# Kernel tuning notes

Measured on AMD Instinct MI355X. Metric: run time of the kernel, lower is better.

## Reference

```python
import jax, jax.numpy as jnp
import numpy as np

NEG_SLOPE = 0.2  # PyG GATConv default leaky_relu slope


def gat_conv(x, src, dst, W, a_src, a_dst, b, heads, out_dim):
    """PyG-style GATConv (add_self_loops already applied to src/dst, concat=True)."""
    N = x.shape[0]
    h = (x @ W).reshape(N, heads, out_dim)              # [N,H,D]
    alpha_s = jnp.sum(h * a_src, axis=-1)               # [N,H]
    alpha_d = jnp.sum(h * a_dst, axis=-1)               # [N,H]
    e = jax.nn.leaky_relu(alpha_s[src] + alpha_d[dst], NEG_SLOPE)  # [E,H]
    # segment softmax over destination node neighborhoods
    m = jax.lax.stop_gradient(jax.ops.segment_max(e, dst, num_segments=N))
    ex = jnp.exp(e - m[dst])
    denom = jax.ops.segment_sum(ex, dst, num_segments=N)
    alpha = ex / denom[dst]                              # [E,H]
    msg = h[src] * alpha[..., None]                      # [E,H,D]
    out = jax.ops.segment_sum(msg, dst, num_segments=N)  # [N,H,D]
    return out.reshape(N, heads * out_dim) + b


def setup_inputs() -> dict:
    key = jax.random.key(0)
    ks = jax.random.split(key, 12)
    N, E, C_IN, HID, HEADS, C_OUT = 50000, 800000, 128, 64, 4, 64
    x = jax.random.normal(ks[0], (N, C_IN), dtype=jnp.float32)
    edge_index = jax.random.randint(ks[1], (2, E), 0, N, dtype=jnp.int32)
    s1 = 1.0 / np.sqrt(C_IN)
    s2 = 1.0 / np.sqrt(HID * HEADS)
    return {
        "x": x,
        "edge_index": edge_index,
        "W1": jax.random.normal(ks[2], (C_IN, HEADS * HID), jnp.float32) * s1,
        "a_src1": jax.random.normal(ks[3], (HEADS, HID), jnp.float32) * s1,
        "a_dst1": jax.random.normal(ks[4], (HEADS, HID), jnp.float32) * s1,
        "b1": jnp.zeros((HEADS * HID,), jnp.float32),
        "W2": jax.random.normal(ks[5], (HEADS * HID, C_OUT), jnp.float32) * s2,
        "a_src2": jax.random.normal(ks[6], (1, C_OUT), jnp.float32) * s2,
        "a_dst2": jax.random.normal(ks[7], (1, C_OUT), jnp.float32) * s2,
        "b2": jnp.zeros((C_OUT,), jnp.float32),
    }


def reference(x, edge_index, W1, a_src1, a_dst1, b1, W2, a_src2, a_dst2, b2):
    N = x.shape[0]
    loop = jnp.arange(N, dtype=edge_index.dtype)
    src = jnp.concatenate([edge_index[0], loop])  # add self-loops (PyG default)
    dst = jnp.concatenate([edge_index[1], loop])
    # dropout layers are identity in eval mode
    h = gat_conv(x, src, dst, W1, a_src1, a_dst1, b1, heads=4, out_dim=64)
    h = jax.nn.relu(h)
    out = gat_conv(h, src, dst, W2, a_src2, a_dst2, b2, heads=1, out_dim=64)
    return out  # [N, out_channels]
```

## Files before the change

### kernel.cpp

```cpp
#include <hip/hip_runtime.h>
#include <math.h>

#define LEAKY 0.2f
#define SB 256
#define FTILE 4096

typedef _Float16 half2v __attribute__((ext_vector_type(2)));
typedef _Float16 half4 __attribute__((ext_vector_type(4)));
typedef _Float16 half8 __attribute__((ext_vector_type(8)));
typedef float f32x4 __attribute__((ext_vector_type(4)));

static inline int ceil_div(int a, int b) { return (a + b - 1) / b; }

__device__ __forceinline__ int PERM(int p) {
  int q = p & 63;
  return (p & ~63) | (((q & 3) << 4) | (q >> 2));
}

__global__ __launch_bounds__(256) void k_zero(int4* __restrict__ buf, int n4) {
  int i = blockIdx.x * 256 + threadIdx.x;
  if (i < n4) buf[i] = make_int4(0, 0, 0, 0);
}

__global__ __launch_bounds__(256) void k_fillA(const int* __restrict__ ei,
                                               int* __restrict__ bcnt,
                                               int2* __restrict__ pairs,
                                               int NE, int N, int chunk, int cap) {
  __shared__ int hist[256], base[256], cnt2[256];
  int t = threadIdx.x;
  hist[t] = 0;
  cnt2[t] = 0;
  __syncthreads();
  int ET = NE + N;
  int e0 = blockIdx.x * FTILE;
  int sv[16], dv[16];
#pragma unroll
  for (int j = 0; j < 16; ++j) {
    int e = e0 + t + 256 * j;
    if (e < ET) {
      sv[j] = (e < NE) ? ei[e] : (e - NE);
      dv[j] = (e < NE) ? ei[NE + e] : (e - NE);
      atomicAdd(&hist[dv[j] / chunk], 1);
    } else {
      dv[j] = -1;
    }
  }
  __syncthreads();
  if (hist[t] > 0) base[t] = t * cap + atomicAdd(&bcnt[t], hist[t]);
  __syncthreads();
#pragma unroll
  for (int j = 0; j < 16; ++j) {
    if (dv[j] >= 0) {
      int b = dv[j] / chunk;
      int r = atomicAdd(&cnt2[b], 1);
      pairs[base[b] + r] = make_int2(dv[j], sv[j]);
    }
  }
}

__global__ __launch_bounds__(256) void k_bscan(const int* __restrict__ bcnt,
                                               int* __restrict__ bpre,
                                               int* __restrict__ off, int N) {
  __shared__ int s[256];
  int t = threadIdx.x;
  int v = bcnt[t];
  s[t] = v;
  __syncthreads();
  for (int o = 1; o < 256; o <<= 1) {
    int u = (t >= o) ? s[t - o] : 0;
    __syncthreads();
    s[t] += u;
    __syncthreads();
  }
  bpre[t] = s[t] - v;
  if (t == 255) off[N] = s[255];
}

__global__ __launch_bounds__(256) void k_fillB2(const int2* __restrict__ pairs,
                                                const int* __restrict__ bcnt,
                                                const int* __restrict__ bpre,
                                                int* __restrict__ off,
                                                int* __restrict__ csr, int N,
                                                int chunk, int cap) {
  __shared__ int hist[256], cur[256];
  int b = blockIdx.x, t = threadIdx.x;
  int node0 = b * chunk;
  hist[t] = 0;
  __syncthreads();
  int i0 = b * cap, i1 = i0 + bcnt[b];
  for (int i = i0 + t; i < i1; i += 256)
    atomicAdd(&hist[pairs[i].x - node0], 1);
  __syncthreads();
  int v = hist[t];
  for (int o = 1; o < 256; o <<= 1) {
    int u = (t >= o) ? hist[t - o] : 0;
    __syncthreads();
    hist[t] += u;
    __syncthreads();
  }
  int ex = hist[t] - v + bpre[b];
  if (t < chunk && node0 + t < N) off[node0 + t] = ex;
  cur[t] = ex;
  __syncthreads();
  for (int i = i0 + t; i < i1; i += 256) {
    int2 pr = pairs[i];
    int pos = atomicAdd(&cur[pr.x - node0], 1);
    csr[pos] = pr.y;
  }
}

__global__ __launch_bounds__(256) void k_prep(const float* __restrict__ W1,
                                              const float* __restrict__ W2,
                                              const float* __restrict__ a_src1,
                                              const float* __restrict__ a_dst1,
                                              const float* __restrict__ a_src2,
                                              const float* __restrict__ a_dst2,
                                              const float* __restrict__ b1,
                                              _Float16* __restrict__ w1hf,
                                              _Float16* __restrict__ w2f,
                                              float* __restrict__ wt1s,
                                              float* __restrict__ wt1d,
                                              float* __restrict__ b1p) {
  int idx = blockIdx.x * 256 + threadIdx.x;
  if (idx < 32768) {
    int i = idx & 7, l = (idx >> 3) & 63, ct = (idx >> 9) & 3, ks = (idx >> 11) & 3,
        h = idx >> 13;
    int k = 32 * ks + 8 * (l >> 4) + i;
    int col = h * 64 + 16 * ct + (l & 15);
    w1hf[idx] = (_Float16)W1[k * 256 + col];
    return;
  }
  int i2 = idx - 32768;
  if (i2 < 16384) {
    int i = i2 & 7, l = (i2 >> 3) & 63, ct = (i2 >> 9) & 3, ks = i2 >> 11;
    int kp = 32 * ks + 8 * (l >> 4) + i;
    int col = 16 * ct + (l & 15);
    w2f[i2] = (_Float16)W2[PERM(kp) * 64 + col];
    return;
  }
  int i3 = i2 - 16384;
  if (i3 < 512) {
    int h = i3 & 3, k = i3 >> 2;
    float ss = 0.f, sd = 0.f;
    for (int d = 0; d < 64; ++d) {
      float wv = W1[k * 256 + h * 64 + d];
      ss = fmaf(wv, a_src1[h * 64 + d], ss);
      sd = fmaf(wv, a_dst1[h * 64 + d], sd);
    }
    wt1s[i3] = ss;
    wt1d[i3] = sd;
    return;
  }
  int i4 = i3 - 512;
  if (i4 < 256) b1p[i4] = b1[PERM(i4)];
}

__global__ __launch_bounds__(256) void k_logits1(const float* __restrict__ x,
                                                 const float* __restrict__ wt1s,
                                                 const float* __restrict__ wt1d,
                                                 _Float16* __restrict__ x16,
                                                 float* __restrict__ as1,
                                                 float* __restrict__ ad1, int N) {
  int w = threadIdx.x >> 6, l = threadIdx.x & 63;
  int n = blockIdx.x * 4 + w;
  if (n >= N) return;
  float2 xv = *reinterpret_cast<const float2*>(x + (size_t)n * 128 + 2 * l);
  half2v xh;
  xh[0] = (_Float16)xv.x;
  xh[1] = (_Float16)xv.y;
  *reinterpret_cast<half2v*>(x16 + (size_t)n * 128 + 2 * l) = xh;
  float4 w0s = reinterpret_cast<const float4*>(wt1s)[2 * l];
  float4 w1s = reinterpret_cast<const float4*>(wt1s)[2 * l + 1];
  float4 w0d = reinterpret_cast<const float4*>(wt1d)[2 * l];
  float4 w1d = reinterpret_cast<const float4*>(wt1d)[2 * l + 1];
  float sa[4], sd[4];
  sa[0] = xv.x * w0s.x + xv.y * w1s.x;
  sa[1] = xv.x * w0s.y + xv.y * w1s.y;
  sa[2] = xv.x * w0s.z + xv.y * w1s.z;
  sa[3] = xv.x * w0s.w + xv.y * w1s.w;
  sd[0] = xv.x * w0d.x + xv.y * w1d.x;
  sd[1] = xv.x * w0d.y + xv.y * w1d.y;
  sd[2] = xv.x * w0d.z + xv.y * w1d.z;
  sd[3] = xv.x * w0d.w + xv.y * w1d.w;
#pragma unroll
  for (int o = 1; o <= 32; o <<= 1) {
#pragma unroll
    for (int h = 0; h < 4; ++h) {
      sa[h] += __shfl_xor(sa[h], o, 64);
      sd[h] += __shfl_xor(sd[h], o, 64);
    }
  }
  if (l == 0) {
#pragma unroll
    for (int h = 0; h < 4; ++h) {
      as1[n * 4 + h] = sa[h];
      ad1[n * 4 + h] = sd[h];
    }
  }
}

__global__ __launch_bounds__(256) void k_alpha1(const float* __restrict__ as1,
                                                const float* __restrict__ ad1,
                                                const int* __restrict__ off,
                                                const int* __restrict__ csr,
                                                _Float16* __restrict__ alpha,
                                                float* __restrict__ linv1, int N) {
  int w = threadIdx.x >> 6, lane = threadIdx.x & 63;
  int n = blockIdx.x * 4 + w;
  if (n >= N) return;
  int eidx = lane >> 2, h = lane & 3;
  float adv = ad1[n * 4 + h];
  int e0 = off[n], e1 = off[n + 1];
  float m = -INFINITY;
  for (int base = e0; base < e1; base += 16) {
    int idx = base + eidx;
    if (idx < e1) {
      int s = csr[idx];
      float t = as1[s * 4 + h] + adv;
      t = t > 0.f ? t : LEAKY * t;
      m = fmaxf(m, t);
    }
  }
#pragma unroll
  for (int o = 4; o <= 32; o <<= 1) m = fmaxf(m, __shfl_xor(m, o, 64));
  float lp = 0.f;
  for (int base = e0; base < e1; base += 16) {
    int idx = base + eidx;
    if (idx < e1) {
      int s = csr[idx];
      float t = as1[s * 4 + h] + adv;
      t = t > 0.f ? t : LEAKY * t;
      float p = __expf(t - m);
      alpha[(size_t)idx * 4 + h] = (_Float16)p;
      lp += p;
    }
  }
#pragma unroll
  for (int o = 4; o <= 32; o <<= 1) lp += __shfl_xor(lp, o, 64);
  if (lane < 4) linv1[n * 4 + h] = 1.f / lp;
}

__global__ __launch_bounds__(256) void k_xagg(const _Float16* __restrict__ x16,
                                              const _Float16* __restrict__ alpha,
                                              const float* __restrict__ linv1,
                                              const int* __restrict__ off,
                                              const int* __restrict__ csr,
                                              _Float16* __restrict__ xagg, int N) {
  int w = threadIdx.x >> 6, l = threadIdx.x & 63;
  int n = blockIdx.x * 4 + w;
  if (n >= N) return;
  int slot = l >> 4, kq = l & 15;
  int e0 = off[n], e1 = off[n + 1];
  half2v acc[4][4];
#pragma unroll
  for (int h = 0; h < 4; ++h)
#pragma unroll
    for (int j = 0; j < 4; ++j) acc[h][j] = (half2v){(_Float16)0.f, (_Float16)0.f};
  const _Float16 zero16 = (_Float16)0.f;
  for (int base = e0; base < e1; base += 16) {
#pragma unroll
    for (int u = 0; u < 4; ++u) {
      int e = base + 4 * u + slot;
      int ec = min(e, e1 - 1);
      int src = csr[ec];
      half4 al = *reinterpret_cast<const half4*>(alpha + (size_t)ec * 4);
      if (e >= e1) al = (half4){zero16, zero16, zero16, zero16};
      half8 hv = *reinterpret_cast<const half8*>(x16 + (size_t)src * 128 + 8 * kq);
      half2v xp[4];
      xp[0] = (half2v){hv[0], hv[1]};
      xp[1] = (half2v){hv[2], hv[3]};
      xp[2] = (half2v){hv[4], hv[5]};
      xp[3] = (half2v){hv[6], hv[7]};
#pragma unroll
      for (int h = 0; h < 4; ++h) {
        half2v ah = (half2v){al[h], al[h]};
#pragma unroll
        for (int j = 0; j < 4; ++j) acc[h][j] = ah * xp[j] + acc[h][j];
      }
    }
  }
#pragma unroll
  for (int h = 0; h < 4; ++h)
#pragma unroll
    for (int j = 0; j < 4; ++j) {
      int v0 = __shfl_xor(__builtin_bit_cast(int, acc[h][j]), 16, 64);
      acc[h][j] = acc[h][j] + __builtin_bit_cast(half2v, v0);
      int v1 = __shfl_xor(__builtin_bit_cast(int, acc[h][j]), 32, 64);
      acc[h][j] = acc[h][j] + __builtin_bit_cast(half2v, v1);
    }
  if (slot == 0) {
    float4 linv = *reinterpret_cast<const float4*>(linv1 + n * 4);
    float rin[4] = {linv.x, linv.y, linv.z, linv.w};
#pragma unroll
    for (int h = 0; h < 4; ++h) {
      half8 o;
#pragma unroll
      for (int j = 0; j < 4; ++j) {
        o[2 * j] = (_Float16)((float)acc[h][j][0] * rin[h]);
        o[2 * j + 1] = (_Float16)((float)acc[h][j][1] * rin[h]);
      }
      *reinterpret_cast<half8*>(xagg + (size_t)n * 512 + h * 128 + 8 * kq) = o;
    }
  }
}

__global__ __launch_bounds__(256) void k_gemm12(const _Float16* __restrict__ xagg,
                                                const _Float16* __restrict__ w1hf,
                                                const _Float16* __restrict__ w2f,
                                                const float* __restrict__ b1p,
                                                const float* __restrict__ a_src2,
                                                const float* __restrict__ a_dst2,
                                                _Float16* __restrict__ h2p,
                                                float* __restrict__ as2,
                                                float* __restrict__ ad2, int N) {
  __shared__ _Float16 hs[64 * 256];
  int w = threadIdx.x >> 6, l = threadIdx.x & 63;
  int n0 = blockIdx.x * 64 + 16 * w;
  int lrow = l & 15, lgrp = l >> 4;
  int arow = min(n0 + lrow, N - 1);
  f32x4 acc1[4][4];
#pragma unroll
  for (int h = 0; h < 4; ++h)
#pragma unroll
    for (int ct = 0; ct < 4; ++ct) acc1[h][ct] = (f32x4){0.f, 0.f, 0.f, 0.f};
#pragma unroll
  for (int h = 0; h < 4; ++h) {
#pragma unroll
    for (int ks = 0; ks < 4; ++ks) {
      half8 af = *reinterpret_cast<const half8*>(xagg + (size_t)arow * 512 + h * 128 +
                                                 32 * ks + 8 * lgrp);
      const half8* bp =
          reinterpret_cast<const half8*>(w1hf) + (size_t)((h * 4 + ks) * 4) * 64 + l;
#pragma unroll
      for (int ct = 0; ct < 4; ++ct) {
        half8 bf = bp[ct * 64];
        acc1[h][ct] = __builtin_amdgcn_mfma_f32_16x16x32_f16(af, bf, acc1[h][ct], 0, 0, 0);
      }
    }
  }
  int lr0 = 16 * w + 4 * lgrp;
#pragma unroll
  for (int h = 0; h < 4; ++h) {
    float4 bv = *reinterpret_cast<const float4*>(b1p + h * 64 + lrow * 4);
#pragma unroll
    for (int r = 0; r < 4; ++r) {
      int row = lr0 + r;
      half4 o;
      o[0] = (_Float16)fmaxf(acc1[h][0][r] + bv.x, 0.f);
      o[1] = (_Float16)fmaxf(acc1[h][1][r] + bv.y, 0.f);
      o[2] = (_Float16)fmaxf(acc1[h][2][r] + bv.z, 0.f);
      o[3] = (_Float16)fmaxf(acc1[h][3][r] + bv.w, 0.f);
      int ba = row * 512 + ((h * 128 + lrow * 8) ^ ((row & 7) << 4));
      *reinterpret_cast<half4*>(reinterpret_cast<char*>(hs) + ba) = o;
    }
  }
  __syncthreads();
  int arow2 = 16 * w + lrow;
  f32x4 acc2[4];
#pragma unroll
  for (int ct = 0; ct < 4; ++ct) acc2[ct] = (f32x4){0.f, 0.f, 0.f, 0.f};
#pragma unroll
  for (int ks = 0; ks < 8; ++ks) {
    int ba = arow2 * 512 + ((64 * ks + 16 * lgrp) ^ ((arow2 & 7) << 4));
    half8 af = *reinterpret_cast<const half8*>(reinterpret_cast<const char*>(hs) + ba);
    const half8* bp = reinterpret_cast<const half8*>(w2f) + (size_t)(ks * 4) * 64 + l;
#pragma unroll
    for (int ct = 0; ct < 4; ++ct) {
      half8 bf = bp[ct * 64];
      acc2[ct] = __builtin_amdgcn_mfma_f32_16x16x32_f16(af, bf, acc2[ct], 0, 0, 0);
    }
  }
  float ascol[4], adcol[4];
#pragma unroll
  for (int ct = 0; ct < 4; ++ct) {
    ascol[ct] = a_src2[16 * ct + lrow];
    adcol[ct] = a_dst2[16 * ct + lrow];
  }
  int rbase = n0 + 4 * lgrp;
#pragma unroll
  for (int r = 0; r < 4; ++r) {
    int row = rbase + r;
    bool ok = row < N;
    float sa = 0.f, sd = 0.f;
    half4 o;
#pragma unroll
    for (int ct = 0; ct < 4; ++ct) {
      float v = acc2[ct][r];
      o[ct] = (_Float16)v;
      sa = fmaf(v, ascol[ct], sa);
      sd = fmaf(v, adcol[ct], sd);
    }
    if (ok) *reinterpret_cast<half4*>(h2p + (size_t)row * 64 + lrow * 4) = o;
#pragma unroll
    for (int oo = 1; oo <= 8; oo <<= 1) {
      sa += __shfl_xor(sa, oo, 64);
      sd += __shfl_xor(sd, oo, 64);
    }
    if (ok && lrow == 0) {
      as2[row] = sa;
      ad2[row] = sd;
    }
  }
}

__global__ __launch_bounds__(256) void k_agg2(const _Float16* __restrict__ h2p,
                                              const float* __restrict__ as2,
                                              const float* __restrict__ ad2,
                                              const float* __restrict__ b2,
                                              const int* __restrict__ off,
                                              const int* __restrict__ csr,
                                              float* __restrict__ out, int N) {
  int w = threadIdx.x >> 6, lane = threadIdx.x & 63;
  int n = blockIdx.x * 4 + w;
  if (n >= N) return;
  float adv = ad2[n];
  int e0 = off[n], e1 = off[n + 1];
  float m = -INFINITY;
  for (int idx = e0 + lane; idx < e1; idx += 64) {
    float t = as2[csr[idx]] + adv;
    t = t > 0.f ? t : LEAKY * t;
    m = fmaxf(m, t);
  }
#pragma unroll
  for (int o = 1; o <= 32; o <<= 1) m = fmaxf(m, __shfl_xor(m, o, 64));
  int slot = lane >> 3, q = lane & 7;
  float acc[8];
  float lp = 0.f;
#pragma unroll
  for (int k = 0; k < 8; ++k) acc[k] = 0.f;
  for (int base = e0; base < e1; base += 16) {
#pragma unroll
    for (int u = 0; u < 2; ++u) {
      int e = base + 8 * u + slot;
      int ec = min(e, e1 - 1);
      int s = csr[ec];
      float t = as2[s] + adv;
      t = t > 0.f ? t : LEAKY * t;
      float p = (e < e1) ? __expf(t - m) : 0.f;
      lp += p;
      half8 hv = *reinterpret_cast<const half8*>(h2p + (size_t)s * 64 + 8 * q);
#pragma unroll
      for (int k = 0; k < 8; ++k) acc[k] = fmaf(p, (float)hv[k], acc[k]);
    }
  }
#pragma unroll
  for (int o = 8; o <= 32; o <<= 1) {
    lp += __shfl_xor(lp, o, 64);
#pragma unroll
    for (int k = 0; k < 8; ++k) acc[k] += __shfl_xor(acc[k], o, 64);
  }
  if (slot == 0) {
    float rinv = 1.f / lp;
#pragma unroll
    for (int k = 0; k < 8; ++k) {
      int col = ((k & 3) << 4) + 2 * q + (k >> 2);
      out[(size_t)n * 64 + col] = acc[k] * rinv + b2[col];
    }
  }
}

extern "C" void kernel_launch(void* const* d_in, const int* in_sizes, int n_in,
                              void* d_out, int out_size, void* d_ws, size_t ws_size,
                              hipStream_t stream) {
  const float* x = (const float*)d_in[0];
  const int* ei = (const int*)d_in[1];
  const float* W1 = (const float*)d_in[2];
  const float* a_src1 = (const float*)d_in[3];
  const float* a_dst1 = (const float*)d_in[4];
  const float* b1 = (const float*)d_in[5];
  const float* W2 = (const float*)d_in[6];
  const float* a_src2 = (const float*)d_in[7];
  const float* a_dst2 = (const float*)d_in[8];
  const float* b2 = (const float*)d_in[9];
  float* out = (float*)d_out;

  const int N = in_sizes[0] / 128;
  const int NE = in_sizes[1] / 2;
  const int ET = NE + N;
  const int chunk = ceil_div(N, SB);
  const int cap = 3 * ceil_div(ET, SB);

  char* p = (char*)d_ws;
  auto alloc = [&](size_t bytes) {
    char* r = p;
    p += (bytes + 255) & ~(size_t)255;
    return r;
  };
  int* bcnt = (int*)alloc((size_t)SB * 4);
  int* bpre = (int*)alloc((size_t)SB * 4);
  int* off = (int*)alloc((size_t)(N + 1) * 4);
  int* csr = (int*)alloc((size_t)ET * 4);
  int2* pairs = (int2*)alloc((size_t)SB * cap * 8);
  _Float16* w1hf = (_Float16*)alloc((size_t)32768 * 2);
  _Float16* w2f = (_Float16*)alloc((size_t)16384 * 2);
  float* wt1s = (float*)alloc((size_t)512 * 4);
  float* wt1d = (float*)alloc((size_t)512 * 4);
  float* b1p = (float*)alloc((size_t)256 * 4);
  _Float16* x16 = (_Float16*)alloc((size_t)N * 128 * 2);
  _Float16* xagg = (_Float16*)alloc((size_t)N * 512 * 2);
  float* as1 = (float*)alloc((size_t)N * 4 * 4);
  float* ad1 = (float*)alloc((size_t)N * 4 * 4);
  _Float16* alpha1 = (_Float16*)alloc((size_t)ET * 4 * 2);
  float* linv1 = (float*)alloc((size_t)N * 4 * 4);
  _Float16* h2p = x16;
  float* as2 = (float*)alloc((size_t)N * 4);
  float* ad2 = (float*)alloc((size_t)N * 4);

  k_zero<<<1, 256, 0, stream>>>((int4*)bcnt, SB / 4);
  k_fillA<<<ceil_div(ET, FTILE), 256, 0, stream>>>(ei, bcnt, pairs, NE, N, chunk, cap);
  k_bscan<<<1, 256, 0, stream>>>(bcnt, bpre, off, N);
  k_fillB2<<<SB, 256, 0, stream>>>(pairs, bcnt, bpre, off, csr, N, chunk, cap);
  k_prep<<<198, 256, 0, stream>>>(W1, W2, a_src1, a_dst1, a_src2, a_dst2, b1,
                                  w1hf, w2f, wt1s, wt1d, b1p);

  k_logits1<<<ceil_div(N, 4), 256, 0, stream>>>(x, wt1s, wt1d, x16, as1, ad1, N);
  k_alpha1<<<ceil_div(N, 4), 256, 0, stream>>>(as1, ad1, off, csr, alpha1, linv1, N);
  k_xagg<<<ceil_div(N, 4), 256, 0, stream>>>(x16, alpha1, linv1, off, csr, xagg, N);
  k_gemm12<<<ceil_div(N, 64), 256, 0, stream>>>(xagg, w1hf, w2f, b1p, a_src2,
                                                a_dst2, h2p, as2, ad2, N);
  k_agg2<<<ceil_div(N, 4), 256, 0, stream>>>(h2p, as2, ad2, b2, off, csr, out, N);
}
```

Baseline: 185.1 us.

## Pack CSR build pairs into 32 bits, fuse bucket scan, unroll gathers deeper

The bucketed CSR build now stores each (local dst, src) pair as one 32-bit word (20-bit src, local dst in the high bits), halving pair traffic. k_fillA re-reads edge indices in a second pass instead of holding them in registers. The separate k_bscan launch is removed: every k_fillB2 block recomputes the 256-bucket prefix scan itself. The edge loops in k_xagg and k_agg2 are unrolled twice as deep for more memory-level parallelism, at the cost of more registers. The packing assumes node ids fit in 20 bits.

After: 193.0 us. +4.2%, slower.

```diff
diff --git a/kernel.cpp b/kernel.cpp
--- a/kernel.cpp
+++ b/kernel.cpp
@@ -24,7 +24,7 @@
 
 __global__ __launch_bounds__(256) void k_fillA(const int* __restrict__ ei,
                                                int* __restrict__ bcnt,
-                                               int2* __restrict__ pairs,
+                                               unsigned* __restrict__ pairs,
                                                int NE, int N, int chunk, int cap) {
   __shared__ int hist[256], base[256], cnt2[256];
   int t = threadIdx.x;
@@ -33,63 +33,48 @@
   __syncthreads();
   int ET = NE + N;
   int e0 = blockIdx.x * FTILE;
-  int sv[16], dv[16];
-#pragma unroll
-  for (int j = 0; j < 16; ++j) {
-    int e = e0 + t + 256 * j;
-    if (e < ET) {
-      sv[j] = (e < NE) ? ei[e] : (e - NE);
-      dv[j] = (e < NE) ? ei[NE + e] : (e - NE);
-      atomicAdd(&hist[dv[j] / chunk], 1);
-    } else {
-      dv[j] = -1;
-    }
+  int e1 = min(e0 + FTILE, ET);
+  for (int e = e0 + t; e < e1; e += 256) {
+    int d = (e < NE) ? ei[NE + e] : (e - NE);
+    atomicAdd(&hist[d / chunk], 1);
   }
   __syncthreads();
   if (hist[t] > 0) base[t] = t * cap + atomicAdd(&bcnt[t], hist[t]);
   __syncthreads();
-#pragma unroll
-  for (int j = 0; j < 16; ++j) {
-    if (dv[j] >= 0) {
-      int b = dv[j] / chunk;
-      int r = atomicAdd(&cnt2[b], 1);
-      pairs[base[b] + r] = make_int2(dv[j], sv[j]);
-    }
-  }
-}
-
-__global__ __launch_bounds__(256) void k_bscan(const int* __restrict__ bcnt,
-                                               int* __restrict__ bpre,
-                                               int* __restrict__ off, int N) {
-  __shared__ int s[256];
-  int t = threadIdx.x;
-  int v = bcnt[t];
-  s[t] = v;
-  __syncthreads();
-  for (int o = 1; o < 256; o <<= 1) {
-    int u = (t >= o) ? s[t - o] : 0;
-    __syncthreads();
-    s[t] += u;
-    __syncthreads();
-  }
-  bpre[t] = s[t] - v;
-  if (t == 255) off[N] = s[255];
-}
-
-__global__ __launch_bounds__(256) void k_fillB2(const int2* __restrict__ pairs,
+  for (int e = e0 + t; e < e1; e += 256) {
+    int s = (e < NE) ? ei[e] : (e - NE);
+    int d = (e < NE) ? ei[NE + e] : (e - NE);
+    int b = d / chunk;
+    int r = atomicAdd(&cnt2[b], 1);
+    pairs[base[b] + r] = ((unsigned)(d - b * chunk) << 20) | (unsigned)s;
+  }
+}
+
+__global__ __launch_bounds__(256) void k_fillB2(const unsigned* __restrict__ pairs,
                                                 const int* __restrict__ bcnt,
-                                                const int* __restrict__ bpre,
                                                 int* __restrict__ off,
                                                 int* __restrict__ csr, int N,
                                                 int chunk, int cap) {
-  __shared__ int hist[256], cur[256];
+  __shared__ int sc[256], hist[256], cur[256];
   int b = blockIdx.x, t = threadIdx.x;
   int node0 = b * chunk;
+  int bv = bcnt[t];
+  sc[t] = bv;
+  __syncthreads();
+  for (int o = 1; o < 256; o <<= 1) {
+    int u = (t >= o) ? sc[t - o] : 0;
+    __syncthreads();
+    sc[t] += u;
+    __syncthreads();
+  }
+  int bpre_b = sc[b] - bcnt[b];
+  int total = sc[255];
+  if (t == 0 && b == (N - 1) / chunk) off[N] = total;
   hist[t] = 0;
   __syncthreads();
   int i0 = b * cap, i1 = i0 + bcnt[b];
   for (int i = i0 + t; i < i1; i += 256)
-    atomicAdd(&hist[pairs[i].x - node0], 1);
+    atomicAdd(&hist[pairs[i] >> 20], 1);
   __syncthreads();
   int v = hist[t];
   for (int o = 1; o < 256; o <<= 1) {
@@ -98,14 +83,14 @@
     hist[t] += u;
     __syncthreads();
   }
-  int ex = hist[t] - v + bpre[b];
+  int ex = hist[t] - v + bpre_b;
   if (t < chunk && node0 + t < N) off[node0 + t] = ex;
   cur[t] = ex;
   __syncthreads();
   for (int i = i0 + t; i < i1; i += 256) {
-    int2 pr = pairs[i];
-    int pos = atomicAdd(&cur[pr.x - node0], 1);
-    csr[pos] = pr.y;
+    unsigned u = pairs[i];
+    int pos = atomicAdd(&cur[u >> 20], 1);
+    csr[pos] = (int)(u & 0xFFFFFu);
   }
 }
 
@@ -257,9 +242,9 @@
 #pragma unroll
     for (int j = 0; j < 4; ++j) acc[h][j] = (half2v){(_Float16)0.f, (_Float16)0.f};
   const _Float16 zero16 = (_Float16)0.f;
-  for (int base = e0; base < e1; base += 16) {
-#pragma unroll
-    for (int u = 0; u < 4; ++u) {
+  for (int base = e0; base < e1; base += 32) {
+#pragma unroll
+    for (int u = 0; u < 8; ++u) {
       int e = base + 4 * u + slot;
       int ec = min(e, e1 - 1);
       int src = csr[ec];
@@ -428,9 +413,9 @@
   float lp = 0.f;
 #pragma unroll
   for (int k = 0; k < 8; ++k) acc[k] = 0.f;
-  for (int base = e0; base < e1; base += 16) {
-#pragma unroll
-    for (int u = 0; u < 2; ++u) {
+  for (int base = e0; base < e1; base += 32) {
+#pragma unroll
+    for (int u = 0; u < 4; ++u) {
       int e = base + 8 * u + slot;
       int ec = min(e, e1 - 1);
       int s = csr[ec];
@@ -487,10 +472,9 @@
     return r;
   };
   int* bcnt = (int*)alloc((size_t)SB * 4);
-  int* bpre = (int*)alloc((size_t)SB * 4);
   int* off = (int*)alloc((size_t)(N + 1) * 4);
   int* csr = (int*)alloc((size_t)ET * 4);
-  int2* pairs = (int2*)alloc((size_t)SB * cap * 8);
+  unsigned* pairs = (unsigned*)alloc((size_t)SB * cap * 4);
   _Float16* w1hf = (_Float16*)alloc((size_t)32768 * 2);
   _Float16* w2f = (_Float16*)alloc((size_t)16384 * 2);
   float* wt1s = (float*)alloc((size_t)512 * 4);
@@ -508,8 +492,7 @@
 
   k_zero<<<1, 256, 0, stream>>>((int4*)bcnt, SB / 4);
   k_fillA<<<ceil_div(ET, FTILE), 256, 0, stream>>>(ei, bcnt, pairs, NE, N, chunk, cap);
-  k_bscan<<<1, 256, 0, stream>>>(bcnt, bpre, off, N);
-  k_fillB2<<<SB, 256, 0, stream>>>(pairs, bcnt, bpre, off, csr, N, chunk, cap);
+  k_fillB2<<<SB, 256, 0, stream>>>(pairs, bcnt, off, csr, N, chunk, cap);
   k_prep<<<198, 256, 0, stream>>>(W1, W2, a_src1, a_dst1, a_src2, a_dst2, b1,
                                   w1hf, w2f, wt1s, wt1d, b1p);
 
```
